# Performance work log

Measured on AMD Instinct MI355X. Metric: run time of the kernel, lower is better.

Reference implementation:

```python
import jax, jax.numpy as jnp
import numpy as np

NUM_HEADS = 4
LN_EPS = 1e-5
ALPHA_SCALE = 2.0


def setup_inputs() -> dict:
    key = jax.random.key(0)
    ks = jax.random.split(key, 8)
    bs, C, H, W = 64, 256, 56, 56
    T, D = 6, 192
    HW = H * W
    w = lambda k, shape: (jax.random.normal(k, shape, jnp.float32) * 0.02)
    return {
        "features": jax.random.normal(ks[0], (bs, C, H, W), jnp.float32),
        "tokens": jax.random.normal(ks[1], (T, bs, D), jnp.float32),
        # mlp: Linear(HW -> T)
        "mlp_w": w(ks[2], (T, HW)), "mlp_b": jnp.zeros((T,), jnp.float32),
        # q: Linear(D -> C)
        "q_w": w(ks[3], (C, D)), "q_b": jnp.zeros((C,), jnp.float32),
        # alpha: Linear(D -> C)
        "alpha_w": w(ks[4], (C, D)), "alpha_b": jnp.zeros((C,), jnp.float32),
        # proj: Linear(C -> D)
        "proj_w": w(ks[5], (D, C)), "proj_b": jnp.zeros((D,), jnp.float32),
        "ln_g": jnp.ones((D,), jnp.float32), "ln_b": jnp.zeros((D,), jnp.float32),
    }


def reference(features, tokens, mlp_w, mlp_b, q_w, q_b,
              alpha_w, alpha_b, proj_w, proj_b, ln_g, ln_b):
    bs, C, H, W = features.shape
    T, _, D = tokens.shape
    h = NUM_HEADS
    dh = C // h
    HW = H * W
    scale = dh ** -0.5

    f = features.reshape(bs, C, HW)

    # mlp branch: Linear over HW -> [bs, C, T] -> permute to [T, bs, C]
    t_sum = jnp.einsum('bcn,tn->tbc', f, mlp_w) + mlp_b[:, None, None]

    # attn branch: few tokens attend over H*W feature map (k reused as v)
    q = jnp.einsum('tbd,cd->tbc', tokens, q_w) + q_b          # [T, bs, C]
    q = q.reshape(T, bs, h, dh).transpose(1, 2, 0, 3)         # [bs, h, T, dh]
    k = f.reshape(bs, h, dh, HW)                              # [bs, h, dh, HW]
    attn = jnp.einsum('bhtd,bhdn->bhtn', q, k) * scale        # [bs, h, T, HW]
    a = jax.nn.softmax(attn, axis=-1)
    attn_out = jnp.einsum('bhtn,bhdn->bhtd', a, k)            # [bs, h, T, dh]
    t_a = attn_out.transpose(2, 0, 1, 3).reshape(T, bs, C)
    t_sum = t_sum + t_a

    # dynamic gate: h_sigmoid(alpha(tokens)) * 2.0
    alp = jnp.clip(jnp.einsum('tbd,cd->tbc', tokens, alpha_w) + alpha_b + 3.0,
                   0.0, 6.0) / 6.0 * ALPHA_SCALE              # [T, bs, C]
    t_sum = t_sum * alp

    # proj + residual + LayerNorm (post-norm, drop_path rate 0 -> identity)
    t_sum = jnp.einsum('tbc,dc->tbd', t_sum, proj_w) + proj_b  # [T, bs, D]
    tok = tokens + t_sum
    mu = tok.mean(-1, keepdims=True)
    var = ((tok - mu) ** 2).mean(-1, keepdims=True)
    tok = (tok - mu) * jax.lax.rsqrt(var + LN_EPS) * ln_g + ln_b

    return tok, attn.reshape(bs, h, T, H, W)
```

## Files before the change

kernel.cpp:

```cpp
#include <hip/hip_runtime.h>
#include <hip/hip_bf16.h>

constexpr int BS = 64, C = 256, NH = 4, DH = 64, T = 6, D = 192;
constexpr int HW = 3136;
constexpr int NT = 64;
constexpr int S = 7, CPB = 7;
constexpr int PNF = 72;
constexpr int PNS = 68;
constexpr int QP = 72;
constexpr float SCALE = 0.125f;
constexpr float LN_EPS = 1e-5f;

typedef short bf16x8 __attribute__((ext_vector_type(8)));
typedef float f32x4 __attribute__((ext_vector_type(4)));

__device__ inline unsigned short f2bf(float x) {
    union { float f; unsigned u; } v; v.f = x;
    unsigned r = v.u + 0x7FFFu + ((v.u >> 16) & 1u);
    return (unsigned short)(r >> 16);
}

__device__ inline void st_bf8(unsigned short* dst, float4 p) {
    unsigned lo = (unsigned)f2bf(p.x) | ((unsigned)f2bf(p.y) << 16);
    unsigned hi = (unsigned)f2bf(p.z) | ((unsigned)f2bf(p.w) << 16);
    *(uint2*)dst = make_uint2(lo, hi);
}

__device__ inline int fsw(int r, int n) { return n ^ (((r >> 3) & 3) << 4); }

__device__ inline void wg_barrier_lgkm() {
    asm volatile("s_waitcnt lgkmcnt(0)" ::: "memory");
    __builtin_amdgcn_s_barrier();
    asm volatile("" ::: "memory");
}

__global__ __launch_bounds__(256) void qalpha_kernel(
    const float* __restrict__ tokens,
    const float* __restrict__ q_w,
    const float* __restrict__ q_b,
    const float* __restrict__ alpha_w,
    const float* __restrict__ alpha_b,
    float* __restrict__ q_ws,
    float* __restrict__ alp_ws)
{
    int b = blockIdx.x;
    int c = threadIdx.x;
    __shared__ float tok_s[T][D];
    for (int i = c; i < T * (D / 4); i += 256) {
        int t = i / (D / 4), v = i % (D / 4);
        *(float4*)&tok_s[t][4 * v] =
            *(const float4*)&tokens[((size_t)t * BS + b) * D + 4 * v];
    }
    __syncthreads();

    const float4* qr = (const float4*)(q_w + (size_t)c * D);
    const float4* ar = (const float4*)(alpha_w + (size_t)c * D);
    float accq[T] = {0, 0, 0, 0, 0, 0};
    float acca[T] = {0, 0, 0, 0, 0, 0};
    for (int v = 0; v < D / 4; ++v) {
        float4 qw4 = qr[v], aw4 = ar[v];
#pragma unroll
        for (int t = 0; t < T; ++t) {
            float4 t4 = *(const float4*)&tok_s[t][4 * v];
            accq[t] += qw4.x * t4.x + qw4.y * t4.y + qw4.z * t4.z + qw4.w * t4.w;
            acca[t] += aw4.x * t4.x + aw4.y * t4.y + aw4.z * t4.z + aw4.w * t4.w;
        }
    }
    float qb = q_b[c], ab = alpha_b[c];
#pragma unroll
    for (int t = 0; t < T; ++t) {
        size_t idx = ((size_t)t * BS + b) * C + c;
        q_ws[idx] = accq[t] + qb;
        float aa = acca[t] + ab + 3.0f;
        alp_ws[idx] = fminf(fmaxf(aa, 0.0f), 6.0f) * (2.0f / 6.0f);
    }
}

struct PF { float4 f0, f1, f2, f3, m; };

__global__ __launch_bounds__(256) void fused_attn_mlp(
    const float* __restrict__ feat,
    const float* __restrict__ mlp_w,
    const float* __restrict__ q_ws,
    float* __restrict__ out_attn,
    float* __restrict__ o_part,
    float* __restrict__ mlp_part,
    float* __restrict__ ml_part)
{
    int bh = blockIdx.x / S, sp = blockIdx.x % S;
    int b = bh / NH, h = bh % NH;
    int tid = threadIdx.x;
    int wave = tid >> 6, lane = tid & 63;
    int col = lane & 15, quad = lane >> 4;

    __shared__ unsigned short fch[DH][PNF];
    __shared__ unsigned short pw[16][PNF];
    __shared__ unsigned short qs[16][QP];
    __shared__ float st[T][PNS];
    __shared__ float m_s[T], l_s[T], al_s[T];

    const float* fbase = feat + ((size_t)b * C + h * DH) * HW;
    float* obase = out_attn + ((size_t)bh * T) * HW;

    const int o0 = (tid / 16) * HW + 4 * (tid % 16);
    const int o1 = ((tid + 256) / 16) * HW + 4 * ((tid + 256) % 16);
    const int o2 = ((tid + 512) / 16) * HW + 4 * ((tid + 512) % 16);
    const int o3 = ((tid + 768) / 16) * HW + 4 * ((tid + 768) % 16);

    auto pf_issue = [&](PF& p, int n0) {
        p.f0 = *(const float4*)&fbase[o0 + n0];
        p.f1 = *(const float4*)&fbase[o1 + n0];
        p.f2 = *(const float4*)&fbase[o2 + n0];
        p.f3 = *(const float4*)&fbase[o3 + n0];
        if (tid < 96) p.m = *(const float4*)&mlp_w[o0 + n0];
    };
    auto pf_commit = [&](const PF& p) {
        int r0 = tid / 16,         c0 = 4 * (tid % 16);
        int r1 = (tid + 256) / 16, c1 = 4 * ((tid + 256) % 16);
        int r2 = (tid + 512) / 16, c2 = 4 * ((tid + 512) % 16);
        int r3 = (tid + 768) / 16, c3 = 4 * ((tid + 768) % 16);
        st_bf8(&fch[r0][fsw(r0, c0)], p.f0);
        st_bf8(&fch[r1][fsw(r1, c1)], p.f1);
        st_bf8(&fch[r2][fsw(r2, c2)], p.f2);
        st_bf8(&fch[r3][fsw(r3, c3)], p.f3);
        if (tid < 96) {
            int rm = 6 + tid / 16, cm = 4 * (tid % 16);
            st_bf8(&pw[rm][fsw(rm, cm)], p.m);
        }
    };

    const int nsp = sp * CPB * NT;
    PF A;
    pf_issue(A, nsp);

    for (int i = tid; i < 4 * PNF; i += 256) pw[12 + i / PNF][i % PNF] = 0;
    if (tid < T) { m_s[tid] = -3e38f; l_s[tid] = 0.f; }
    for (int i = tid; i < T * DH; i += 256) {
        int t = i / DH, c2 = i % DH;
        qs[t][c2] = f2bf(q_ws[((size_t)t * BS + b) * C + h * DH + c2]);
    }

    f32x4 accPW = {0.f, 0.f, 0.f, 0.f};
    wg_barrier_lgkm();

#pragma unroll 1
    for (int cc = 0; cc < CPB; ++cc) {
        const int n0 = nsp + cc * NT;

        pf_commit(A);
        if (cc + 1 < CPB) pf_issue(A, n0 + NT);
        wg_barrier_lgkm();

        {
            int tile = wave;
            bf16x8 a0 = *(const bf16x8*)&qs[col][quad * 8];
            bf16x8 a1 = *(const bf16x8*)&qs[col][32 + quad * 8];
            int nsw = (tile * 16 + col) ^ (quad << 4);
            bf16x8 b0, b1;
#pragma unroll
            for (int j = 0; j < 8; ++j) {
                b0[j] = (short)fch[quad * 8 + j][nsw];
                b1[j] = (short)fch[32 + quad * 8 + j][nsw];
            }
            f32x4 acc = {0.f, 0.f, 0.f, 0.f};
            acc = __builtin_amdgcn_mfma_f32_16x16x32_bf16(a0, b0, acc, 0, 0, 0);
            acc = __builtin_amdgcn_mfma_f32_16x16x32_bf16(a1, b1, acc, 0, 0, 0);
#pragma unroll
            for (int reg = 0; reg < 4; ++reg) {
                int r = quad * 4 + reg;
                if (r < 6) st[r][tile * 16 + col] = acc[reg] * SCALE;
            }
        }
        wg_barrier_lgkm();

        for (int t = wave; t < T; t += 4) {
            float v0 = st[t][lane];
            float mloc = v0;
#pragma unroll
            for (int off = 32; off; off >>= 1) mloc = fmaxf(mloc, __shfl_down(mloc, off));
            mloc = __shfl(mloc, 0);
            float m_old = m_s[t], m_new = fmaxf(m_old, mloc);
            float p0 = __expf(v0 - m_new);
            pw[t][lane] = f2bf(p0);
            float ssum = p0;
#pragma unroll
            for (int off = 32; off; off >>= 1) ssum += __shfl_down(ssum, off);
            if (lane == 0) {
                float alpha = __expf(m_old - m_new);
                l_s[t] = l_s[t] * alpha + ssum;
                m_s[t] = m_new;
                al_s[t] = alpha;
            }
            if (lane < NT / 4) {
                *(float4*)&obase[(size_t)t * HW + n0 + 4 * lane] =
                    *(const float4*)&st[t][4 * lane];
            }
        }
        wg_barrier_lgkm();

        {
            float alpha = (col < 6) ? al_s[col] : 1.0f;
            accPW *= alpha;
            int ra = wave * 16 + col;
#pragma unroll
            for (int ks = 0; ks < 2; ++ks) {
                bf16x8 af = *(const bf16x8*)&fch[ra][fsw(ra, ks * 32 + quad * 8)];
                bf16x8 bf = *(const bf16x8*)&pw[col][fsw(col, ks * 32 + quad * 8)];
                accPW = __builtin_amdgcn_mfma_f32_16x16x32_bf16(af, bf, accPW, 0, 0, 0);
            }
        }
        wg_barrier_lgkm();
    }

    {
#pragma unroll
        for (int reg = 0; reg < 4; ++reg) {
            int c2 = wave * 16 + quad * 4 + reg;
            if (col < 6) {
                o_part[((size_t)blockIdx.x * T + col) * DH + c2] = accPW[reg];
            } else if (col < 12) {
                mlp_part[((size_t)blockIdx.x * T + (col - 6)) * DH + c2] = accPW[reg];
            }
        }
    }
    if (tid < 2 * T) {
        int t = tid >> 1;
        ml_part[((size_t)blockIdx.x * T + t) * 2 + (tid & 1)] =
            (tid & 1) ? l_s[t] : m_s[t];
    }
}

__global__ __launch_bounds__(256) void merge_proj_ln_kernel(
    const float* __restrict__ o_part,
    const float* __restrict__ mlp_part,
    const float* __restrict__ ml_part,
    const float* __restrict__ mlp_b,
    const float* __restrict__ alp_ws,
    const float* __restrict__ tokens,
    const float* __restrict__ proj_w,
    const float* __restrict__ proj_b,
    const float* __restrict__ ln_g,
    const float* __restrict__ ln_b,
    float* __restrict__ out_tok)
{
    int tb = blockIdx.x;
    int t = tb / BS, b = tb % BS;
    int tid = threadIdx.x;
    __shared__ float g_s[C];
    __shared__ float r1[4], r2[4];

    {
        int c = tid;
        int h = c >> 6, cl = c & 63;
        int bh = b * NH + h;
        float m[S], l[S];
        float M = -3e38f;
#pragma unroll
        for (int s = 0; s < S; ++s) {
            size_t blk = (size_t)(bh * S + s);
            m[s] = ml_part[(blk * T + t) * 2 + 0];
            l[s] = ml_part[(blk * T + t) * 2 + 1];
            M = fmaxf(M, m[s]);
        }
        float L = 0.f, O = 0.f, MLP = 0.f;
#pragma unroll
        for (int s = 0; s < S; ++s) {
            float w = __expf(m[s] - M);
            size_t blk = (size_t)(bh * S + s);
            size_t pidx = (blk * T + t) * DH + cl;
            L += l[s] * w;
            O += o_part[pidx] * w;
            MLP += mlp_part[pidx];
        }
        size_t idx = (size_t)tb * C + c;
        g_s[c] = (MLP + mlp_b[t] + O / L) * alp_ws[idx];
    }
    __syncthreads();

    if (tid < D) {
        int d = tid;
        float acc = proj_b[d] + tokens[(size_t)tb * D + d];
        const float4* pr = (const float4*)(proj_w + (size_t)d * C);
#pragma unroll 8
        for (int v = 0; v < C / 4; ++v) {
            float4 w4 = pr[v];
            float4 g4 = *(const float4*)&g_s[4 * v];
            acc += w4.x * g4.x + w4.y * g4.y + w4.z * g4.z + w4.w * g4.w;
        }

        float s1 = acc, s2 = acc * acc;
#pragma unroll
        for (int off = 32; off; off >>= 1) { s1 += __shfl_down(s1, off); s2 += __shfl_down(s2, off); }
        int wv = d >> 6, lane = d & 63;
        if (lane == 0) { r1[wv] = s1; r2[wv] = s2; }
        __syncthreads();
        float sum1 = r1[0] + r1[1] + r1[2];
        float sum2 = r2[0] + r2[1] + r2[2];
        float mu = sum1 * (1.0f / D);
        float var = sum2 * (1.0f / D) - mu * mu;
        float inv = rsqrtf(var + LN_EPS);
        out_tok[(size_t)tb * D + d] = (acc - mu) * inv * ln_g[d] + ln_b[d];
    } else {
        __syncthreads();
    }
}

extern "C" void kernel_launch(void* const* d_in, const int* in_sizes, int n_in,
                              void* d_out, int out_size, void* d_ws, size_t ws_size,
                              hipStream_t stream) {
    const float* features = (const float*)d_in[0];
    const float* tokens   = (const float*)d_in[1];
    const float* mlp_w    = (const float*)d_in[2];
    const float* mlp_b    = (const float*)d_in[3];
    const float* q_w      = (const float*)d_in[4];
    const float* q_b      = (const float*)d_in[5];
    const float* alpha_w  = (const float*)d_in[6];
    const float* alpha_b  = (const float*)d_in[7];
    const float* proj_w   = (const float*)d_in[8];
    const float* proj_b   = (const float*)d_in[9];
    const float* ln_g     = (const float*)d_in[10];
    const float* ln_b     = (const float*)d_in[11];

    float* out_tok  = (float*)d_out;
    float* out_attn = (float*)d_out + T * BS * D;

    constexpr int NBLK = BS * NH * S;
    float* q_ws     = (float*)d_ws;
    float* alp_ws   = q_ws + T * BS * C;
    float* ml_part  = alp_ws + T * BS * C;
    float* o_part   = ml_part + NBLK * T * 2;
    float* mlp_part = o_part + NBLK * T * DH;

    qalpha_kernel<<<BS, 256, 0, stream>>>(
        tokens, q_w, q_b, alpha_w, alpha_b, q_ws, alp_ws);

    fused_attn_mlp<<<NBLK, 256, 0, stream>>>(
        features, mlp_w, q_ws, out_attn, o_part, mlp_part, ml_part);

    merge_proj_ln_kernel<<<T * BS, 256, 0, stream>>>(
        o_part, mlp_part, ml_part, mlp_b, alp_ws, tokens,
        proj_w, proj_b, ln_g, ln_b, out_tok);
}
```

Before: 350.5 us.

## Run fused attention block as a single wave and drop workgroup barriers

Rewrites the fused attention+MLP kernel from a 4-wave 256-thread block to a single 64-lane wavefront per block. The one wave now does all four MFMA column tiles, all six softmax rows and all loads itself, so every s_barrier can be removed. Each lane holds 16 float4 prefetch registers instead of 4, which raises register pressure and may lower occupancy. The grid keeps the same block count, so per-CU parallelism now has to come from more resident small blocks. LDS hazards between waves no longer exist, and within the wave the code relies on LDS ordering.

After: 354.8 us. Within noise of the previous version (+1.2%).

```diff
diff --git a/kernel.cpp b/kernel.cpp
--- a/kernel.cpp
+++ b/kernel.cpp
@@ -27,12 +27,6 @@
 }
 
 __device__ inline int fsw(int r, int n) { return n ^ (((r >> 3) & 3) << 4); }
-
-__device__ inline void wg_barrier_lgkm() {
-    asm volatile("s_waitcnt lgkmcnt(0)" ::: "memory");
-    __builtin_amdgcn_s_barrier();
-    asm volatile("" ::: "memory");
-}
 
 __global__ __launch_bounds__(256) void qalpha_kernel(
     const float* __restrict__ tokens,
@@ -76,9 +70,7 @@
     }
 }
 
-struct PF { float4 f0, f1, f2, f3, m; };
-
-__global__ __launch_bounds__(256) void fused_attn_mlp(
+__global__ __launch_bounds__(64) void fused_attn_mlp(
     const float* __restrict__ feat,
     const float* __restrict__ mlp_w,
     const float* __restrict__ q_ws,
@@ -89,72 +81,65 @@
 {
     int bh = blockIdx.x / S, sp = blockIdx.x % S;
     int b = bh / NH, h = bh % NH;
-    int tid = threadIdx.x;
-    int wave = tid >> 6, lane = tid & 63;
+    int lane = threadIdx.x;
     int col = lane & 15, quad = lane >> 4;
 
     __shared__ unsigned short fch[DH][PNF];
     __shared__ unsigned short pw[16][PNF];
     __shared__ unsigned short qs[16][QP];
     __shared__ float st[T][PNS];
-    __shared__ float m_s[T], l_s[T], al_s[T];
+    __shared__ float m_s[8], l_s[8], al_s[16];
 
     const float* fbase = feat + ((size_t)b * C + h * DH) * HW;
+    const float* fl  = fbase + (size_t)quad * HW + 4 * col;
+    const float* ml0 = mlp_w + (size_t)quad * HW + 4 * col;
+    const float* ml1 = mlp_w + (size_t)(4 + (quad & 1)) * HW + 4 * col;
     float* obase = out_attn + ((size_t)bh * T) * HW;
 
-    const int o0 = (tid / 16) * HW + 4 * (tid % 16);
-    const int o1 = ((tid + 256) / 16) * HW + 4 * ((tid + 256) % 16);
-    const int o2 = ((tid + 512) / 16) * HW + 4 * ((tid + 512) % 16);
-    const int o3 = ((tid + 768) / 16) * HW + 4 * ((tid + 768) % 16);
-
-    auto pf_issue = [&](PF& p, int n0) {
-        p.f0 = *(const float4*)&fbase[o0 + n0];
-        p.f1 = *(const float4*)&fbase[o1 + n0];
-        p.f2 = *(const float4*)&fbase[o2 + n0];
-        p.f3 = *(const float4*)&fbase[o3 + n0];
-        if (tid < 96) p.m = *(const float4*)&mlp_w[o0 + n0];
+    float4 pf[16];
+    float4 pm0, pm1;
+
+    auto pf_issue = [&](int n0) {
+#pragma unroll
+        for (int i = 0; i < 16; ++i)
+            pf[i] = *(const float4*)&fl[(size_t)(4 * i) * HW + n0];
+        pm0 = *(const float4*)&ml0[n0];
+        if (lane < 32) pm1 = *(const float4*)&ml1[n0];
     };
-    auto pf_commit = [&](const PF& p) {
-        int r0 = tid / 16,         c0 = 4 * (tid % 16);
-        int r1 = (tid + 256) / 16, c1 = 4 * ((tid + 256) % 16);
-        int r2 = (tid + 512) / 16, c2 = 4 * ((tid + 512) % 16);
-        int r3 = (tid + 768) / 16, c3 = 4 * ((tid + 768) % 16);
-        st_bf8(&fch[r0][fsw(r0, c0)], p.f0);
-        st_bf8(&fch[r1][fsw(r1, c1)], p.f1);
-        st_bf8(&fch[r2][fsw(r2, c2)], p.f2);
-        st_bf8(&fch[r3][fsw(r3, c3)], p.f3);
-        if (tid < 96) {
-            int rm = 6 + tid / 16, cm = 4 * (tid % 16);
-            st_bf8(&pw[rm][fsw(rm, cm)], p.m);
-        }
+    auto pf_commit = [&]() {
+#pragma unroll
+        for (int i = 0; i < 16; ++i) {
+            int r = 4 * i + quad;
+            st_bf8(&fch[r][fsw(r, 4 * col)], pf[i]);
+        }
+        { int rm = 6 + quad; st_bf8(&pw[rm][fsw(rm, 4 * col)], pm0); }
+        if (lane < 32) { int rm = 10 + quad; st_bf8(&pw[rm][fsw(rm, 4 * col)], pm1); }
     };
 
     const int nsp = sp * CPB * NT;
-    PF A;
-    pf_issue(A, nsp);
-
-    for (int i = tid; i < 4 * PNF; i += 256) pw[12 + i / PNF][i % PNF] = 0;
-    if (tid < T) { m_s[tid] = -3e38f; l_s[tid] = 0.f; }
-    for (int i = tid; i < T * DH; i += 256) {
-        int t = i / DH, c2 = i % DH;
-        qs[t][c2] = f2bf(q_ws[((size_t)t * BS + b) * C + h * DH + c2]);
-    }
-
-    f32x4 accPW = {0.f, 0.f, 0.f, 0.f};
-    wg_barrier_lgkm();
+    pf_issue(nsp);
+
+    for (int i = lane; i < 4 * PNF; i += 64) pw[12 + i / PNF][i % PNF] = 0;
+    if (lane < T) { m_s[lane] = -3e38f; l_s[lane] = 0.f; }
+#pragma unroll
+    for (int t = 0; t < T; ++t)
+        qs[t][lane] = f2bf(q_ws[((size_t)t * BS + b) * C + h * DH + lane]);
+    bf16x8 a0 = *(const bf16x8*)&qs[col][quad * 8];
+    bf16x8 a1 = *(const bf16x8*)&qs[col][32 + quad * 8];
+
+    f32x4 acc[4];
+#pragma unroll
+    for (int ct = 0; ct < 4; ++ct) acc[ct] = (f32x4){0.f, 0.f, 0.f, 0.f};
 
 #pragma unroll 1
     for (int cc = 0; cc < CPB; ++cc) {
         const int n0 = nsp + cc * NT;
 
-        pf_commit(A);
-        if (cc + 1 < CPB) pf_issue(A, n0 + NT);
-        wg_barrier_lgkm();
-
-        {
-            int tile = wave;
-            bf16x8 a0 = *(const bf16x8*)&qs[col][quad * 8];
-            bf16x8 a1 = *(const bf16x8*)&qs[col][32 + quad * 8];
+        pf_commit();
+        if (cc + 1 < CPB) pf_issue(n0 + NT);
+
+#pragma unroll
+        for (int tile = 0; tile < 4; ++tile) {
             int nsw = (tile * 16 + col) ^ (quad << 4);
             bf16x8 b0, b1;
 #pragma unroll
@@ -162,71 +147,69 @@
                 b0[j] = (short)fch[quad * 8 + j][nsw];
                 b1[j] = (short)fch[32 + quad * 8 + j][nsw];
             }
-            f32x4 acc = {0.f, 0.f, 0.f, 0.f};
-            acc = __builtin_amdgcn_mfma_f32_16x16x32_bf16(a0, b0, acc, 0, 0, 0);
-            acc = __builtin_amdgcn_mfma_f32_16x16x32_bf16(a1, b1, acc, 0, 0, 0);
+            f32x4 sa = {0.f, 0.f, 0.f, 0.f};
+            sa = __builtin_amdgcn_mfma_f32_16x16x32_bf16(a0, b0, sa, 0, 0, 0);
+            sa = __builtin_amdgcn_mfma_f32_16x16x32_bf16(a1, b1, sa, 0, 0, 0);
 #pragma unroll
             for (int reg = 0; reg < 4; ++reg) {
                 int r = quad * 4 + reg;
-                if (r < 6) st[r][tile * 16 + col] = acc[reg] * SCALE;
-            }
-        }
-        wg_barrier_lgkm();
-
-        for (int t = wave; t < T; t += 4) {
-            float v0 = st[t][lane];
-            float mloc = v0;
-#pragma unroll
-            for (int off = 32; off; off >>= 1) mloc = fmaxf(mloc, __shfl_down(mloc, off));
-            mloc = __shfl(mloc, 0);
+                if (r < 6) st[r][tile * 16 + col] = sa[reg] * SCALE;
+            }
+        }
+
+#pragma unroll
+        for (int t = 0; t < T; ++t) {
+            float v = st[t][lane];
+            float mloc = v;
+#pragma unroll
+            for (int off = 32; off; off >>= 1) mloc = fmaxf(mloc, __shfl_xor(mloc, off));
             float m_old = m_s[t], m_new = fmaxf(m_old, mloc);
-            float p0 = __expf(v0 - m_new);
-            pw[t][lane] = f2bf(p0);
-            float ssum = p0;
-#pragma unroll
-            for (int off = 32; off; off >>= 1) ssum += __shfl_down(ssum, off);
+            float p = __expf(v - m_new);
+            pw[t][lane] = f2bf(p);
+            float ssum = p;
+#pragma unroll
+            for (int off = 32; off; off >>= 1) ssum += __shfl_xor(ssum, off);
             if (lane == 0) {
-                float alpha = __expf(m_old - m_new);
-                l_s[t] = l_s[t] * alpha + ssum;
+                float a = __expf(m_old - m_new);
+                al_s[t] = a;
+                l_s[t] = l_s[t] * a + ssum;
                 m_s[t] = m_new;
-                al_s[t] = alpha;
-            }
-            if (lane < NT / 4) {
+            }
+            if (lane < NT / 4)
                 *(float4*)&obase[(size_t)t * HW + n0 + 4 * lane] =
                     *(const float4*)&st[t][4 * lane];
-            }
-        }
-        wg_barrier_lgkm();
-
-        {
-            float alpha = (col < 6) ? al_s[col] : 1.0f;
-            accPW *= alpha;
-            int ra = wave * 16 + col;
+        }
+
+        float alpha = (col < 6) ? al_s[col] : 1.0f;
+#pragma unroll
+        for (int ct = 0; ct < 4; ++ct) {
+            acc[ct] *= alpha;
+            int ra = ct * 16 + col;
 #pragma unroll
             for (int ks = 0; ks < 2; ++ks) {
                 bf16x8 af = *(const bf16x8*)&fch[ra][fsw(ra, ks * 32 + quad * 8)];
                 bf16x8 bf = *(const bf16x8*)&pw[col][fsw(col, ks * 32 + quad * 8)];
-                accPW = __builtin_amdgcn_mfma_f32_16x16x32_bf16(af, bf, accPW, 0, 0, 0);
-            }
-        }
-        wg_barrier_lgkm();
-    }
-
-    {
+                acc[ct] = __builtin_amdgcn_mfma_f32_16x16x32_bf16(af, bf, acc[ct], 0, 0, 0);
+            }
+        }
+    }
+
+#pragma unroll
+    for (int ct = 0; ct < 4; ++ct) {
 #pragma unroll
         for (int reg = 0; reg < 4; ++reg) {
-            int c2 = wave * 16 + quad * 4 + reg;
+            int c2 = ct * 16 + quad * 4 + reg;
             if (col < 6) {
-                o_part[((size_t)blockIdx.x * T + col) * DH + c2] = accPW[reg];
+                o_part[((size_t)blockIdx.x * T + col) * DH + c2] = acc[ct][reg];
             } else if (col < 12) {
-                mlp_part[((size_t)blockIdx.x * T + (col - 6)) * DH + c2] = accPW[reg];
-            }
-        }
-    }
-    if (tid < 2 * T) {
-        int t = tid >> 1;
-        ml_part[((size_t)blockIdx.x * T + t) * 2 + (tid & 1)] =
-            (tid & 1) ? l_s[t] : m_s[t];
+                mlp_part[((size_t)blockIdx.x * T + (col - 6)) * DH + c2] = acc[ct][reg];
+            }
+        }
+    }
+    if (lane < 2 * T) {
+        int t = lane >> 1;
+        ml_part[((size_t)blockIdx.x * T + t) * 2 + (lane & 1)] =
+            (lane & 1) ? l_s[t] : m_s[t];
     }
 }
 
@@ -334,7 +317,7 @@
     qalpha_kernel<<<BS, 256, 0, stream>>>(
         tokens, q_w, q_b, alpha_w, alpha_b, q_ws, alp_ws);
 
-    fused_attn_mlp<<<NBLK, 256, 0, stream>>>(
+    fused_attn_mlp<<<NBLK, 64, 0, stream>>>(
         features, mlp_w, q_ws, out_attn, o_part, mlp_part, ml_part);
 
     merge_proj_ln_kernel<<<T * BS, 256, 0, stream>>>(
```
